# Performance work log

Hardware: AMD Instinct MI355X
Metric: run time of the kernel (lower is better)

Reference implementation:

```python
import jax, jax.numpy as jnp
import numpy as np

PRUNE_RATIO = 0.5
NOISE_SCALE = 0.1
MIXUP_ALPHA = 0.05
TEMPERATURE = 0.5
B, N, D = 32, 4096, 256


def setup_inputs() -> dict:
    key = jax.random.key(0)
    k1, k2, k3 = jax.random.split(key, 3)
    seq = jax.random.normal(k1, (B, N, D), dtype=jnp.float32)
    attn_weights = jax.random.uniform(k2, (B, N), dtype=jnp.float32)
    uniform_noise = jax.random.uniform(k3, (B, N), dtype=jnp.float32)
    return {"seq": seq, "attn_weights": attn_weights, "uniform_noise": uniform_noise}


def reference(seq, attn_weights, uniform_noise):
    b, n, d = seq.shape
    k = max(1, int(n * (1.0 - PRUNE_RATIO)))
    # training branch: gumbel noise from the provided uniform draw
    gumbel = -jnp.log(-jnp.log(uniform_noise + 1e-10) + 1e-10)
    noisy = attn_weights + NOISE_SCALE * gumbel                      # (B, N)
    soft = jax.nn.softmax(noisy / TEMPERATURE, axis=-1)              # (B, N)
    _, top_idx = jax.lax.top_k(soft, k)                              # (B, K) int32
    # gather selected tokens: (B, K, D)
    selected = jnp.take_along_axis(seq, top_idx[:, :, None], axis=1)
    # mixup: mean of the pruned (non-selected) tokens
    mask = jnp.ones((b, n), dtype=seq.dtype).at[
        jnp.arange(b)[:, None], top_idx
    ].set(0.0)                                                       # (B, N), 1 on pruned
    remaining_sum = jnp.einsum('bn,bnd->bd', mask, seq)              # (B, D)
    remaining_count = mask.sum(axis=1, keepdims=True) + 1e-10        # (B, 1)
    remaining_mean = remaining_sum / remaining_count                 # (B, D)
    return selected + MIXUP_ALPHA * remaining_mean[:, None, :]       # (B, K, D)
```

## Files before the change

kernel.cpp:

```cpp
#include <hip/hip_runtime.h>
#include <hip/hip_bf16.h>

#define B_ 32
#define N_ 4096
#define D_ 256
#define K_ 2048
#define SORT_THREADS 1024

__global__ __launch_bounds__(SORT_THREADS) void sort_kernel(
    const float* __restrict__ attn, const float* __restrict__ noise,
    int* __restrict__ sortedIdx, float* __restrict__ meanAccum) {
  __shared__ unsigned long long keys[N_];
  const int b = blockIdx.x;
  const int tid = threadIdx.x;

  for (int i = tid; i < N_; i += SORT_THREADS) {
    float u = noise[b * N_ + i];
    float a = attn[b * N_ + i];
    float x = __fadd_rn(u, 1e-10f);
    float l1 = (float)log((double)x);
    float inner = __fadd_rn(-l1, 1e-10f);
    float g = -(float)log((double)inner);
    float noisy = __fadd_rn(a, __fmul_rn(0.1f, g));
    unsigned int fb = __float_as_uint(noisy);
    fb = (fb & 0x80000000u) ? ~fb : (fb | 0x80000000u);
    keys[i] = ((unsigned long long)fb << 32) | (unsigned int)(~i);
  }
  __syncthreads();

  for (int k = 2; k <= N_; k <<= 1) {
    for (int j = k >> 1; j > 0; j >>= 1) {
      for (int t = tid; t < (N_ / 2); t += SORT_THREADS) {
        int i = ((t & ~(j - 1)) << 1) | (t & (j - 1));
        int ixj = i | j;
        unsigned long long a = keys[i];
        unsigned long long c = keys[ixj];
        bool descSeg = ((i & k) == 0);
        bool doSwap = descSeg ? (a < c) : (a > c);
        if (doSwap) { keys[i] = c; keys[ixj] = a; }
      }
      __syncthreads();
    }
  }

  for (int i = tid; i < N_; i += SORT_THREADS) {
    sortedIdx[b * N_ + i] = (int)(~(unsigned int)(keys[i] & 0xFFFFFFFFu));
  }
  for (int d = tid; d < D_; d += SORT_THREADS) meanAccum[b * D_ + d] = 0.0f;
}

__global__ __launch_bounds__(256) void mean_kernel(
    const float* __restrict__ seq, const int* __restrict__ sortedIdx,
    float* __restrict__ meanAccum) {
  const int b = blockIdx.y;
  const int chunk = blockIdx.x;
  const int tid = threadIdx.x;
  const int dv = tid & 63;
  const int sub = tid >> 6;
  const int base = b * N_ + K_ + chunk * 128;

  float4 acc = make_float4(0.f, 0.f, 0.f, 0.f);
  for (int r = sub; r < 128; r += 4) {
    int idx = sortedIdx[base + r];
    const float4* row = (const float4*)(seq + ((size_t)b * N_ + idx) * D_);
    float4 v = row[dv];
    acc.x += v.x; acc.y += v.y; acc.z += v.z; acc.w += v.w;
  }

  __shared__ float4 red[4][64];
  red[sub][dv] = acc;
  __syncthreads();
  if (sub == 0) {
    float4 s0 = red[0][dv], s1 = red[1][dv], s2 = red[2][dv], s3 = red[3][dv];
    float sx = s0.x + s1.x + s2.x + s3.x;
    float sy = s0.y + s1.y + s2.y + s3.y;
    float sz = s0.z + s1.z + s2.z + s3.z;
    float sw = s0.w + s1.w + s2.w + s3.w;
    float* dst = meanAccum + b * D_ + dv * 4;
    atomicAdd(dst + 0, sx);
    atomicAdd(dst + 1, sy);
    atomicAdd(dst + 2, sz);
    atomicAdd(dst + 3, sw);
  }
}

__global__ __launch_bounds__(256) void out_kernel(
    const float* __restrict__ seq, const int* __restrict__ sortedIdx,
    const float* __restrict__ meanAccum, float* __restrict__ out) {
  const unsigned int t = blockIdx.x * 256u + threadIdx.x;
  const int dv = t & 63;
  const int j = (t >> 6) & (K_ - 1);
  const int b = t >> 17;

  int idx = sortedIdx[b * N_ + j];
  float4 v = ((const float4*)(seq + ((size_t)b * N_ + idx) * D_))[dv];
  float4 m = ((const float4*)(meanAccum + b * D_))[dv];
  const float inv_cnt = 1.0f / 2048.0f;
  float4 o;
  o.x = v.x + 0.05f * (m.x * inv_cnt);
  o.y = v.y + 0.05f * (m.y * inv_cnt);
  o.z = v.z + 0.05f * (m.z * inv_cnt);
  o.w = v.w + 0.05f * (m.w * inv_cnt);
  ((float4*)out)[t] = o;
}

extern "C" void kernel_launch(void* const* d_in, const int* in_sizes, int n_in,
                              void* d_out, int out_size, void* d_ws, size_t ws_size,
                              hipStream_t stream) {
  const float* seq  = (const float*)d_in[0];
  const float* attn = (const float*)d_in[1];
  const float* nois = (const float*)d_in[2];
  float* out = (float*)d_out;

  int* sortedIdx   = (int*)d_ws;
  float* meanAccum = (float*)((char*)d_ws + (size_t)B_ * N_ * 4);

  sort_kernel<<<B_, SORT_THREADS, 0, stream>>>(attn, nois, sortedIdx, meanAccum);
  mean_kernel<<<dim3(16, B_), 256, 0, stream>>>(seq, sortedIdx, meanAccum);
  const int total4 = B_ * K_ * (D_ / 4);
  out_kernel<<<total4 / 256, 256, 0, stream>>>(seq, sortedIdx, meanAccum, out);
}
```

Before: 279.6 us.

## Replace per-batch bitonic sort with parallel rank counting across slices

```diff
diff --git a/kernel.cpp b/kernel.cpp
--- a/kernel.cpp
+++ b/kernel.cpp
@@ -5,16 +5,18 @@
 #define N_ 4096
 #define D_ 256
 #define K_ 2048
-#define SORT_THREADS 1024
+#define RANK_THREADS 512
+#define SLICES 8
 
-__global__ __launch_bounds__(SORT_THREADS) void sort_kernel(
+__global__ __launch_bounds__(RANK_THREADS) void rank_kernel(
     const float* __restrict__ attn, const float* __restrict__ noise,
     int* __restrict__ sortedIdx, float* __restrict__ meanAccum) {
   __shared__ unsigned long long keys[N_];
-  const int b = blockIdx.x;
+  const int b = blockIdx.y;
+  const int slice = blockIdx.x;
   const int tid = threadIdx.x;
 
-  for (int i = tid; i < N_; i += SORT_THREADS) {
+  for (int i = tid; i < N_; i += RANK_THREADS) {
     float u = noise[b * N_ + i];
     float a = attn[b * N_ + i];
     float x = __fadd_rn(u, 1e-10f);
@@ -28,25 +30,20 @@
   }
   __syncthreads();
 
-  for (int k = 2; k <= N_; k <<= 1) {
-    for (int j = k >> 1; j > 0; j >>= 1) {
-      for (int t = tid; t < (N_ / 2); t += SORT_THREADS) {
-        int i = ((t & ~(j - 1)) << 1) | (t & (j - 1));
-        int ixj = i | j;
-        unsigned long long a = keys[i];
-        unsigned long long c = keys[ixj];
-        bool descSeg = ((i & k) == 0);
-        bool doSwap = descSeg ? (a < c) : (a > c);
-        if (doSwap) { keys[i] = c; keys[ixj] = a; }
-      }
-      __syncthreads();
-    }
+  const int i = slice * RANK_THREADS + tid;
+  const unsigned long long mine = keys[i];
+  const ulonglong2* k2 = (const ulonglong2*)keys;
+  unsigned int cnt = 0;
+#pragma unroll 16
+  for (int j = 0; j < N_ / 2; ++j) {
+    ulonglong2 o = k2[j];
+    cnt += (o.x > mine) ? 1u : 0u;
+    cnt += (o.y > mine) ? 1u : 0u;
   }
 
-  for (int i = tid; i < N_; i += SORT_THREADS) {
-    sortedIdx[b * N_ + i] = (int)(~(unsigned int)(keys[i] & 0xFFFFFFFFu));
-  }
-  for (int d = tid; d < D_; d += SORT_THREADS) meanAccum[b * D_ + d] = 0.0f;
+  sortedIdx[b * N_ + (int)cnt] = i;
+
+  if (slice == 0 && tid < D_) meanAccum[b * D_ + tid] = 0.0f;
 }
 
 __global__ __launch_bounds__(256) void mean_kernel(
@@ -115,7 +112,7 @@
   int* sortedIdx   = (int*)d_ws;
   float* meanAccum = (float*)((char*)d_ws + (size_t)B_ * N_ * 4);
 
-  sort_kernel<<<B_, SORT_THREADS, 0, stream>>>(attn, nois, sortedIdx, meanAccum);
+  rank_kernel<<<dim3(SLICES, B_), RANK_THREADS, 0, stream>>>(attn, nois, sortedIdx, meanAccum);
   mean_kernel<<<dim3(16, B_), 256, 0, stream>>>(seq, sortedIdx, meanAccum);
   const int total4 = B_ * K_ * (D_ / 4);
   out_kernel<<<total4 / 256, 256, 0, stream>>>(seq, sortedIdx, meanAccum, out);
```

New measurement: 294.1 us. 5.2% more time.
